# Performance work log

Hardware: AMD Instinct MI355X
Metric: run time of the kernel (lower is better)

## Reference

```python
import jax, jax.numpy as jnp
import numpy as np

N = 50000        # nodes
E = 1_600_000    # edges (avg degree 32)
G = 512          # graphs
F_IN = 9         # node features
H = 64           # hidden dim
ED = 1           # edge feature dim


def _lin(k, fo, fi):
    w = jax.random.normal(k, (fo, fi), jnp.float32) * (1.0 / np.sqrt(fi))
    b = jnp.zeros((fo,), jnp.float32)
    return w, b


def setup_inputs() -> dict:
    key = jax.random.key(0)
    ks = jax.random.split(key, 16)
    x = jax.random.normal(ks[0], (N, F_IN), jnp.float32)
    edge_index = jax.random.randint(ks[1], (2, E), 0, N, dtype=jnp.int64)
    edge_attr = jax.random.normal(ks[2], (E, ED), jnp.float32)
    batch = jnp.sort(jax.random.randint(ks[3], (N,), 0, G, dtype=jnp.int64))
    B_total = jax.random.uniform(ks[4], (G,), jnp.float32) * 100.0
    terminal_mask = jax.random.randint(ks[5], (N,), 0, 2, dtype=jnp.int32)
    c_cost = jax.random.uniform(ks[6], (N,), jnp.float32)
    # conv1: edge lin (ED->F_IN), nn = Linear(F_IN,H), Linear(H,H)
    e1_w, e1_b = _lin(ks[7], F_IN, ED)
    w1a, b1a = _lin(ks[8], H, F_IN)
    w1b, b1b = _lin(ks[9], H, H)
    # conv2: edge lin (ED->H), nn = Linear(H,H), Linear(H,H)
    e2_w, e2_b = _lin(ks[10], H, ED)
    w2a, b2a = _lin(ks[11], H, H)
    w2b, b2b = _lin(ks[12], H, H)
    # readout: Linear(H,H//2), Linear(H//2,1)
    wr1, br1 = _lin(ks[13], H // 2, H)
    wr2, br2 = _lin(ks[14], 1, H // 2)
    return dict(x=x, edge_index=edge_index, edge_attr=edge_attr, batch=batch,
                B_total=B_total, terminal_mask=terminal_mask, c_cost=c_cost,
                e1_w=e1_w, e1_b=e1_b, w1a=w1a, b1a=b1a, w1b=w1b, b1b=b1b,
                e2_w=e2_w, e2_b=e2_b, w2a=w2a, b2a=b2a, w2b=w2b, b2b=b2b,
                wr1=wr1, br1=br1, wr2=wr2, br2=br2)


def _gine(x, src, dst, edge_attr, ew, eb, wa, ba, wb, bb):
    # GINEConv (eps=0): nn(x + sum_j relu(x_j + W_e e_ji))
    e = edge_attr @ ew.T + eb                    # [E, F]
    m = jax.nn.relu(x[src] + e)                  # [E, F] gather + edge fuse
    aggr = jax.ops.segment_sum(m, dst, num_segments=N)  # scatter-add -> [N, F]
    h = x + aggr
    h = jax.nn.relu(h @ wa.T + ba)
    h = jax.nn.relu(h @ wb.T + bb)
    return h


def reference(x, edge_index, edge_attr, batch, B_total, terminal_mask, c_cost,
              e1_w, e1_b, w1a, b1a, w1b, b1b,
              e2_w, e2_b, w2a, b2a, w2b, b2b,
              wr1, br1, wr2, br2):
    src, dst = edge_index[0], edge_index[1]
    h = _gine(x, src, dst, edge_attr, e1_w, e1_b, w1a, b1a, w1b, b1b)
    h = _gine(h, src, dst, edge_attr, e2_w, e2_b, w2a, b2a, w2b, b2b)
    pi_raw = jax.nn.sigmoid((jax.nn.relu(h @ wr1.T + br1) @ wr2.T + br2))[:, 0]
    pi_raw = pi_raw * (1.0 - terminal_mask.astype(jnp.float32))
    node_expenses = pi_raw * c_cost
    total_expenses = jax.ops.segment_sum(node_expenses, batch, num_segments=G)
    ratio = jnp.minimum(B_total[batch] / (total_expenses[batch] + 1e-12), 1.0)
    return pi_raw * ratio
```

## Files before the change

### kernel.cpp

```cpp
#include <hip/hip_runtime.h>
#include <hip/hip_fp16.h>
#include <math.h>

#define N_NODES 50000
#define N_EDGES 1600000
#define N_GRAPHS 512
#define F_IN 9
#define H 64
#define EPB 4096
#define N_SBLK ((N_EDGES + EPB - 1) / EPB)
#define BUCKET_NODES 64
#define N_FBUK ((N_NODES + BUCKET_NODES - 1) / BUCKET_NODES)
#define FCAP 2816

typedef _Float16 f16x8 __attribute__((ext_vector_type(8)));
typedef float f32x4 __attribute__((ext_vector_type(4)));
typedef float f32x2 __attribute__((ext_vector_type(2)));

__device__ __forceinline__ void pack_weights_body(
        const float* __restrict__ w1a, const float* __restrict__ w1b,
        const float* __restrict__ w2a, const float* __restrict__ w2b,
        const float* __restrict__ wr1,
        __half* __restrict__ pk1Ah, __half* __restrict__ pk1Al,
        __half* __restrict__ pk1Bh, __half* __restrict__ pk1Bl,
        __half* __restrict__ pkAh, __half* __restrict__ pkAl,
        __half* __restrict__ pkBh, __half* __restrict__ pkBl,
        __half* __restrict__ pkRh, __half* __restrict__ pkRl) {
    int t = threadIdx.x;
    for (int i = t; i < 2048; i += 512) {
        int j = i & 7, l = (i >> 3) & 63, tt = i >> 9;
        int q = l >> 4, n = l & 15;
        int k = q * 8 + j;
        float v = (k < F_IN) ? w1a[(tt * 16 + n) * F_IN + k] : 0.f;
        __half h = __float2half(v);
        pk1Ah[i] = h; pk1Al[i] = __float2half(v - __half2float(h));
    }
    for (int i = t; i < 4096; i += 512) {
        int j = i & 7, l = (i >> 3) & 63, c = (i >> 9) & 1, tt = i >> 10;
        int q = l >> 4, n = l & 15;
        int src = (tt * 16 + n) * H + c * 32 + q * 8 + j;
        float v1 = w1b[src], wa = w2a[src], wb = w2b[src];
        __half h1 = __float2half(v1), ah = __float2half(wa), bh = __float2half(wb);
        pk1Bh[i] = h1; pk1Bl[i] = __float2half(v1 - __half2float(h1));
        pkAh[i] = ah; pkAl[i] = __float2half(wa - __half2float(ah));
        pkBh[i] = bh; pkBl[i] = __float2half(wb - __half2float(bh));
    }
    for (int i = t; i < 2048; i += 512) {
        int j = i & 7, l = (i >> 3) & 63, c = (i >> 9) & 1, tt = i >> 10;
        int q = l >> 4, n = l & 15;
        float wr = wr1[(tt * 16 + n) * H + c * 32 + q * 8 + j];
        __half rh = __float2half(wr);
        pkRh[i] = rh; pkRl[i] = __float2half(wr - __half2float(rh));
    }
}

__global__ void __launch_bounds__(512)
bucket_scatter(const int* __restrict__ ei,
               const float* __restrict__ ea,
               int* __restrict__ bnext,
               uint2* __restrict__ ebuk,
               const float* __restrict__ w1a,
               const float* __restrict__ w1b,
               const float* __restrict__ w2a,
               const float* __restrict__ w2b,
               const float* __restrict__ wr1,
               __half* pk1Ah, __half* pk1Al,
               __half* pk1Bh, __half* pk1Bl,
               __half* pkAh, __half* pkAl,
               __half* pkBh, __half* pkBl,
               __half* pkRh, __half* pkRl) {
    if (blockIdx.x == 0) {
        pack_weights_body(w1a, w1b, w2a, w2b, wr1, pk1Ah, pk1Al, pk1Bh, pk1Bl,
                          pkAh, pkAl, pkBh, pkBl, pkRh, pkRl);
        return;
    }
    __shared__ int cnt[N_FBUK];
    __shared__ int gbase[N_FBUK];
    for (int i = threadIdx.x; i < N_FBUK; i += 512) cnt[i] = 0;
    __syncthreads();
    int base = (blockIdx.x - 1) * EPB;
    int rk[8];
    unsigned pay[8];
#pragma unroll
    for (int j = 0; j < 8; ++j) {
        int e = base + j * 512 + threadIdx.x;
        rk[j] = -1;
        if (e < N_EDGES) {
            int d = ei[N_EDGES + e];
            int s = ei[e];
            float a = ea[e];
            pay[j] = ((unsigned)s << 16) |
                     (unsigned)__half_as_ushort(__float2half(a));
            int b = d >> 6;
            int r = atomicAdd(&cnt[b], 1);
            rk[j] = (b << 19) | ((d & 63) << 13) | r;
        }
    }
    __syncthreads();
    for (int i = threadIdx.x; i < N_FBUK; i += 512)
        gbase[i] = cnt[i] ? atomicAdd(&bnext[i], cnt[i]) : 0;
    __syncthreads();
#pragma unroll
    for (int j = 0; j < 8; ++j) {
        if (rk[j] < 0) continue;
        int b = rk[j] >> 19, dl = (rk[j] >> 13) & 63, r = rk[j] & 8191;
        int slot = gbase[b] + r;
        if (slot >= FCAP) continue;
        ebuk[(size_t)b * FCAP + slot] = make_uint2(pay[j], (unsigned)dl);
    }
}

#define UNPACK_ATTR(P) __half2float(__ushort_as_half((unsigned short)((P) & 0xffffu)))

__global__ void __launch_bounds__(512)
bucket_fine(const uint2* __restrict__ ebuk,
            const int* __restrict__ bnext,
            unsigned* __restrict__ ep4,
            int* __restrict__ starts, int* __restrict__ deg,
            const float* __restrict__ x,
            const float* __restrict__ e1w,
            const float* __restrict__ e1b,
            float* __restrict__ xs) {
    __shared__ unsigned sorted[FCAP];
    __shared__ int cntN[BUCKET_NODES], offN[BUCKET_NODES], nxtN[BUCKET_NODES];
    int b = blockIdx.x;
    int base = b * FCAP;
    int count = bnext[b];
    if (count > FCAP) count = FCAP;
    int tid = threadIdx.x;
    if (tid < BUCKET_NODES) cntN[tid] = 0;
    __syncthreads();
    uint2 ev[6];
#pragma unroll
    for (int k = 0; k < 6; ++k) {
        int i = tid + k * 512;
        ev[k] = (i < count) ? ebuk[base + i] : make_uint2(0u, 0xFFFFFFFFu);
    }
#pragma unroll
    for (int k = 0; k < 6; ++k)
        if (ev[k].y < (unsigned)BUCKET_NODES) atomicAdd(&cntN[ev[k].y], 1);
    __syncthreads();
    if (tid < 64) {
        int v = cntN[tid];
        int incl = v;
#pragma unroll
        for (int off = 1; off < 64; off <<= 1) {
            int t = __shfl_up(incl, off, 64);
            if (tid >= off) incl += t;
        }
        int excl = incl - v;
        offN[tid] = excl;
        nxtN[tid] = 0;
        int n = (b << 6) + tid;
        if (n < N_NODES) { starts[n] = base + excl; deg[n] = v; }
    }
    __syncthreads();
#pragma unroll
    for (int k = 0; k < 6; ++k) {
        if (ev[k].y < (unsigned)BUCKET_NODES) {
            int r = atomicAdd(&nxtN[ev[k].y], 1);
            sorted[offN[ev[k].y] + r] = ev[k].x;
        }
    }
    __syncthreads();
    for (int i = tid; i < count; i += 512)
        ep4[base + i] = sorted[i];

    int lane = tid & 63, wid = tid >> 6;
    int slot = lane >> 4;
    int f = lane & 15;
    bool act = f < F_IN;
    float wf = act ? e1w[f] : 0.f;
    float bf = act ? e1b[f] : 0.f;
#pragma unroll
    for (int i = 0; i < 8; ++i) {
        int nloc = wid * 8 + i;
        int n = (b << 6) + nloc;
        if (n >= N_NODES) break;
        int off = offN[nloc];
        int dgN = cntN[nloc];
        float acc = 0.f;
        int j = slot;
        for (; j + 12 < dgN; j += 16) {
            unsigned pa = sorted[off + j];
            unsigned pb = sorted[off + j + 4];
            unsigned pc = sorted[off + j + 8];
            unsigned pd = sorted[off + j + 12];
            float xa_ = act ? x[(pa >> 16) * F_IN + f] : 0.f;
            float xb_ = act ? x[(pb >> 16) * F_IN + f] : 0.f;
            float xc_ = act ? x[(pc >> 16) * F_IN + f] : 0.f;
            float xd_ = act ? x[(pd >> 16) * F_IN + f] : 0.f;
            if (act) {
                acc += fmaxf(xa_ + UNPACK_ATTR(pa) * wf + bf, 0.f)
                     + fmaxf(xb_ + UNPACK_ATTR(pb) * wf + bf, 0.f)
                     + fmaxf(xc_ + UNPACK_ATTR(pc) * wf + bf, 0.f)
                     + fmaxf(xd_ + UNPACK_ATTR(pd) * wf + bf, 0.f);
            }
        }
        for (; j < dgN; j += 4) {
            unsigned p = sorted[off + j];
            float xv = act ? x[(p >> 16) * F_IN + f] : 0.f;
            float m = xv + UNPACK_ATTR(p) * wf + bf;
            acc += act ? fmaxf(m, 0.f) : 0.f;
        }
        acc += __shfl_xor(acc, 16, 64);
        acc += __shfl_xor(acc, 32, 64);
        if (lane < 32) {
            float o = (lane < F_IN) ? x[n * F_IN + lane] + acc : 0.f;
            __builtin_nontemporal_store(o, xs + n * 32 + lane);
        }
    }
}

__device__ __forceinline__ void split8(const float* __restrict__ v,
                                       f16x8& hi, f16x8& lo) {
#pragma unroll
    for (int j = 0; j < 8; ++j) {
        _Float16 h = (_Float16)v[j];
        hi[j] = h;
        lo[j] = (_Float16)(v[j] - (float)h);
    }
}

#define TILE3(C, A0H, A0L, A1H, A1L, PH, PL, T) do {                          \
        f16x8 b0h = *(const f16x8*)((PH) + (((T) * 2 + 0) * 64 + lane) * 8);  \
        f16x8 b0l = *(const f16x8*)((PL) + (((T) * 2 + 0) * 64 + lane) * 8);  \
        f16x8 b1h = *(const f16x8*)((PH) + (((T) * 2 + 1) * 64 + lane) * 8);  \
        f16x8 b1l = *(const f16x8*)((PL) + (((T) * 2 + 1) * 64 + lane) * 8);  \
        C = __builtin_amdgcn_mfma_f32_16x16x32_f16(A0H, b0h, C, 0, 0, 0);     \
        C = __builtin_amdgcn_mfma_f32_16x16x32_f16(A0L, b0h, C, 0, 0, 0);     \
        C = __builtin_amdgcn_mfma_f32_16x16x32_f16(A0H, b0l, C, 0, 0, 0);     \
        C = __builtin_amdgcn_mfma_f32_16x16x32_f16(A1H, b1h, C, 0, 0, 0);     \
        C = __builtin_amdgcn_mfma_f32_16x16x32_f16(A1L, b1h, C, 0, 0, 0);     \
        C = __builtin_amdgcn_mfma_f32_16x16x32_f16(A1H, b1l, C, 0, 0, 0);     \
    } while (0)

__global__ void node1_kernel(const float* __restrict__ xs,
                             const __half* __restrict__ pk1Ah, const __half* __restrict__ pk1Al,
                             const float* __restrict__ b1a,
                             const __half* __restrict__ pk1Bh, const __half* __restrict__ pk1Bl,
                             const float* __restrict__ b1b,
                             __half* __restrict__ h1) {
    __shared__ float hbuf[4][16][68];
    int wv = threadIdx.x >> 6;
    int lane = threadIdx.x & 63;
    int gwave = blockIdx.x * 4 + wv;
    bool active = gwave < (N_NODES / 16);
    int base = active ? gwave * 16 : 0;
    int m = lane & 15, q = lane >> 4;
    const _Float16* pAh = (const _Float16*)pk1Ah;
    const _Float16* pAl = (const _Float16*)pk1Al;
    const _Float16* pBh = (const _Float16*)pk1Bh;
    const _Float16* pBl = (const _Float16*)pk1Bl;

    f16x8 ah, al;
    split8(xs + (size_t)(base + m) * 32 + q * 8, ah, al);
#pragma unroll
    for (int t = 0; t < 4; ++t) {
        f32x4 c = {0.f, 0.f, 0.f, 0.f};
        f16x8 bh = *(const f16x8*)(pAh + (t * 64 + lane) * 8);
        f16x8 bl = *(const f16x8*)(pAl + (t * 64 + lane) * 8);
        c = __builtin_amdgcn_mfma_f32_16x16x32_f16(ah, bh, c, 0, 0, 0);
        c = __builtin_amdgcn_mfma_f32_16x16x32_f16(al, bh, c, 0, 0, 0);
        c = __builtin_amdgcn_mfma_f32_16x16x32_f16(ah, bl, c, 0, 0, 0);
        float bias = b1a[t * 16 + m];
#pragma unroll
        for (int r = 0; r < 4; ++r)
            hbuf[wv][q * 4 + r][t * 16 + m] = fmaxf(c[r] + bias, 0.f);
    }
    __syncthreads();
    f16x8 a0h, a0l, a1h, a1l;
    split8(&hbuf[wv][m][q * 8], a0h, a0l);
    split8(&hbuf[wv][m][32 + q * 8], a1h, a1l);
    float tmp[4][4];
#pragma unroll
    for (int t = 0; t < 4; ++t) {
        f32x4 c = {0.f, 0.f, 0.f, 0.f};
        TILE3(c, a0h, a0l, a1h, a1l, pBh, pBl, t);
        float bias = b1b[t * 16 + m];
#pragma unroll
        for (int r = 0; r < 4; ++r)
            tmp[t][r] = fmaxf(c[r] + bias, 0.f);
    }
    __syncthreads();
#pragma unroll
    for (int t = 0; t < 4; ++t)
#pragma unroll
        for (int r = 0; r < 4; ++r)
            hbuf[wv][q * 4 + r][t * 16 + m] = tmp[t][r];
    __syncthreads();
    if (active) {
        int nn = lane >> 2, part = lane & 3;
        f16x8 vlo, vhi;
        const float* rlo = &hbuf[wv][nn][part * 8];
        const float* rhi = &hbuf[wv][nn][32 + part * 8];
#pragma unroll
        for (int j = 0; j < 8; ++j) {
            vlo[j] = (_Float16)rlo[j];
            vhi[j] = (_Float16)rhi[j];
        }
        *(f16x8*)(h1 + (size_t)(base + nn) * 64 + part * 8) = vlo;
        *(f16x8*)(h1 + (size_t)(base + nn) * 64 + 32 + part * 8) = vhi;
    }
}

__global__ void aggphase2_kernel(const __half* __restrict__ h1,
                                 const int* __restrict__ starts,
                                 const int* __restrict__ deg,
                                 const unsigned* __restrict__ ep4,
                                 const float* __restrict__ ew,
                                 const float* __restrict__ eb,
                                 float* __restrict__ htot) {
    int n = blockIdx.x * (blockDim.x >> 6) + (threadIdx.x >> 6);
    int lane = threadIdx.x & 63;
    if (n >= N_NODES) return;
    int q = lane >> 4;
    int l = lane & 15;
    int s0 = starts[n], dg = deg[n];
    const unsigned* ep = ep4 + s0;
    const uint2* h1v = (const uint2*)h1;
    float4 w4 = *(const float4*)(ew + 4 * l);
    float4 b4 = *(const float4*)(eb + 4 * l);
    float a0 = 0.f, a1 = 0.f, a2 = 0.f, a3 = 0.f;
#define EDGE4(P, V) do {                                                   \
        float at = UNPACK_ATTR(P);                                         \
        float2 lo = __half22float2(*(const __half2*)&(V).x);               \
        float2 hi = __half22float2(*(const __half2*)&(V).y);               \
        a0 += fmaxf(lo.x + at * w4.x + b4.x, 0.f);                         \
        a1 += fmaxf(lo.y + at * w4.y + b4.y, 0.f);                         \
        a2 += fmaxf(hi.x + at * w4.z + b4.z, 0.f);                         \
        a3 += fmaxf(hi.y + at * w4.w + b4.w, 0.f);                         \
    } while (0)
    int j = 0;
    for (; j + 16 <= dg; j += 16) {
        unsigned p0 = ep[j + q], p1 = ep[j + 4 + q];
        unsigned p2 = ep[j + 8 + q], p3 = ep[j + 12 + q];
        uint2 v0 = h1v[(size_t)(p0 >> 16) * 16 + l];
        uint2 v1 = h1v[(size_t)(p1 >> 16) * 16 + l];
        uint2 v2 = h1v[(size_t)(p2 >> 16) * 16 + l];
        uint2 v3 = h1v[(size_t)(p3 >> 16) * 16 + l];
        EDGE4(p0, v0); EDGE4(p1, v1); EDGE4(p2, v2); EDGE4(p3, v3);
    }
    for (; j + 4 <= dg; j += 4) {
        unsigned p = ep[j + q];
        uint2 v = h1v[(size_t)(p >> 16) * 16 + l];
        EDGE4(p, v);
    }
    int rem = dg - j;
    if (q < rem) {
        unsigned p = ep[j + q];
        uint2 v = h1v[(size_t)(p >> 16) * 16 + l];
        EDGE4(p, v);
    }
#undef EDGE4
    a0 += __shfl_xor(a0, 16, 64); a0 += __shfl_xor(a0, 32, 64);
    a1 += __shfl_xor(a1, 16, 64); a1 += __shfl_xor(a1, 32, 64);
    a2 += __shfl_xor(a2, 16, 64); a2 += __shfl_xor(a2, 32, 64);
    a3 += __shfl_xor(a3, 16, 64); a3 += __shfl_xor(a3, 32, 64);
    if (q == 0) {
        uint2 sv = h1v[(size_t)n * 16 + l];
        float2 lo = __half22float2(*(const __half2*)&sv.x);
        float2 hi = __half22float2(*(const __half2*)&sv.y);
        f32x4 o;
        o[0] = lo.x + a0; o[1] = lo.y + a1; o[2] = hi.x + a2; o[3] = hi.y + a3;
        __builtin_nontemporal_store(o, (f32x4*)(htot + (size_t)n * 64 + 4 * l));
    }
}

__global__ void node2_kernel(const float* __restrict__ htot,
                             const __half* __restrict__ pkAh, const __half* __restrict__ pkAl,
                             const float* __restrict__ b2a,
                             const __half* __restrict__ pkBh, const __half* __restrict__ pkBl,
                             const float* __restrict__ b2b,
                             const __half* __restrict__ pkRh, const __half* __restrict__ pkRl,
                             const float* __restrict__ br1,
                             const float* __restrict__ wr2,
                             const float* __restrict__ br2,
                             const int* __restrict__ term,
                             const int* __restrict__ batch,
                             const float* __restrict__ ccost,
                             float* __restrict__ pi,
                             float* __restrict__ te) {
    __shared__ float hbuf[4][16][68];
    int wv = threadIdx.x >> 6;
    int lane = threadIdx.x & 63;
    int gwave = blockIdx.x * 4 + wv;
    bool active = gwave < (N_NODES / 16);
    int base = active ? gwave * 16 : 0;
    int m = lane & 15, q = lane >> 4;
    const _Float16* pAh = (const _Float16*)pkAh;
    const _Float16* pAl = (const _Float16*)pkAl;
    const _Float16* pBh = (const _Float16*)pkBh;
    const _Float16* pBl = (const _Float16*)pkBl;
    const _Float16* pRh = (const _Float16*)pkRh;
    const _Float16* pRl = (const _Float16*)pkRl;

    f16x8 a0h, a0l, a1h, a1l;
    {
        const float* hrow = htot + (size_t)(base + m) * 64;
        split8(hrow + q * 8, a0h, a0l);
        split8(hrow + 32 + q * 8, a1h, a1l);
    }
#pragma unroll
    for (int t = 0; t < 4; ++t) {
        f32x4 c = {0.f, 0.f, 0.f, 0.f};
        TILE3(c, a0h, a0l, a1h, a1l, pAh, pAl, t);
        float bias = b2a[t * 16 + m];
#pragma unroll
        for (int r = 0; r < 4; ++r)
            hbuf[wv][q * 4 + r][t * 16 + m] = fmaxf(c[r] + bias, 0.f);
    }
    __syncthreads();
    split8(&hbuf[wv][m][q * 8], a0h, a0l);
    split8(&hbuf[wv][m][32 + q * 8], a1h, a1l);
    float tmp[4][4];
#pragma unroll
    for (int t = 0; t < 4; ++t) {
        f32x4 c = {0.f, 0.f, 0.f, 0.f};
        TILE3(c, a0h, a0l, a1h, a1l, pBh, pBl, t);
        float bias = b2b[t * 16 + m];
#pragma unroll
        for (int r = 0; r < 4; ++r)
            tmp[t][r] = fmaxf(c[r] + bias, 0.f);
    }
    __syncthreads();
#pragma unroll
    for (int t = 0; t < 4; ++t)
#pragma unroll
        for (int r = 0; r < 4; ++r)
            hbuf[wv][q * 4 + r][t * 16 + m] = tmp[t][r];
    __syncthreads();
    split8(&hbuf[wv][m][q * 8], a0h, a0l);
    split8(&hbuf[wv][m][32 + q * 8], a1h, a1l);
    float partial[4] = {0.f, 0.f, 0.f, 0.f};
#pragma unroll
    for (int t = 0; t < 2; ++t) {
        f32x4 c = {0.f, 0.f, 0.f, 0.f};
        TILE3(c, a0h, a0l, a1h, a1l, pRh, pRl, t);
        float bias = br1[t * 16 + m];
        float wv2 = wr2[t * 16 + m];
#pragma unroll
        for (int r = 0; r < 4; ++r)
            partial[r] += fmaxf(c[r] + bias, 0.f) * wv2;
    }
#pragma unroll
    for (int off = 1; off < 16; off <<= 1) {
        partial[0] += __shfl_xor(partial[0], off, 64);
        partial[1] += __shfl_xor(partial[1], off, 64);
        partial[2] += __shfl_xor(partial[2], off, 64);
        partial[3] += __shfl_xor(partial[3], off, 64);
    }
    if (active && m == 0) {
#pragma unroll
        for (int r = 0; r < 4; ++r) {
            int n = base + q * 4 + r;
            float z = partial[r] + br2[0];
            float sig = 1.f / (1.f + expf(-z));
            float pv = sig * (1.f - (float)term[n]);
            pi[n] = pv;
            float contrib = pv * ccost[n];
            if (contrib != 0.f) atomicAdd(&te[batch[n]], contrib);
        }
    }
}

__global__ void final_kernel(const float* __restrict__ pi,
                             const int* __restrict__ batch,
                             const float* __restrict__ Btot,
                             const float* __restrict__ te,
                             float* __restrict__ out) {
    int n = blockIdx.x * blockDim.x + threadIdx.x;
    if (n >= N_NODES) return;
    int b = batch[n];
    float ratio = fminf(Btot[b] / (te[b] + 1e-12f), 1.f);
    out[n] = pi[n] * ratio;
}

extern "C" void kernel_launch(void* const* d_in, const int* in_sizes, int n_in,
                              void* d_out, int out_size, void* d_ws, size_t ws_size,
                              hipStream_t stream) {
    const float* x     = (const float*)d_in[0];
    const int*   ei    = (const int*)d_in[1];
    const float* ea    = (const float*)d_in[2];
    const int*   batch = (const int*)d_in[3];
    const float* Btot  = (const float*)d_in[4];
    const int*   term  = (const int*)d_in[5];
    const float* ccost = (const float*)d_in[6];
    const float* e1w   = (const float*)d_in[7];
    const float* e1b   = (const float*)d_in[8];
    const float* w1a   = (const float*)d_in[9];
    const float* b1a   = (const float*)d_in[10];
    const float* w1b   = (const float*)d_in[11];
    const float* b1b   = (const float*)d_in[12];
    const float* e2w   = (const float*)d_in[13];
    const float* e2b   = (const float*)d_in[14];
    const float* w2a   = (const float*)d_in[15];
    const float* b2a   = (const float*)d_in[16];
    const float* w2b   = (const float*)d_in[17];
    const float* b2b   = (const float*)d_in[18];
    const float* wr1   = (const float*)d_in[19];
    const float* br1   = (const float*)d_in[20];
    const float* wr2   = (const float*)d_in[21];
    const float* br2   = (const float*)d_in[22];

    char* p = (char*)d_ws;
    int*      bnext  = (int*)p;      p += sizeof(int)      * 1024;
    float*    te     = (float*)p;    p += sizeof(float)    * N_GRAPHS;
    int*      starts = (int*)p;      p += sizeof(int)      * N_NODES;
    int*      deg    = (int*)p;      p += sizeof(int)      * N_NODES;
    p = (char*)(((size_t)p + 15) & ~(size_t)15);
    uint2*    ebuk   = (uint2*)p;    p += sizeof(uint2)    * (size_t)N_FBUK * FCAP;
    unsigned* ep4    = (unsigned*)p; p += sizeof(unsigned) * (size_t)N_FBUK * FCAP;
    __half*   h1     = (__half*)p;   p += sizeof(__half)   * (size_t)N_NODES * 64;
    float*    htot   = (float*)p;    p += sizeof(float)    * (size_t)N_NODES * 64;
    float*    xs     = (float*)p;    p += sizeof(float)    * (size_t)N_NODES * 32;
    float*    pi     = (float*)p;    p += sizeof(float)    * N_NODES;
    __half*   pk1Ah  = (__half*)p;   p += sizeof(__half)   * 2048;
    __half*   pk1Al  = (__half*)p;   p += sizeof(__half)   * 2048;
    __half*   pk1Bh  = (__half*)p;   p += sizeof(__half)   * 4096;
    __half*   pk1Bl  = (__half*)p;   p += sizeof(__half)   * 4096;
    __half*   pkAh   = (__half*)p;   p += sizeof(__half)   * 4096;
    __half*   pkAl   = (__half*)p;   p += sizeof(__half)   * 4096;
    __half*   pkBh   = (__half*)p;   p += sizeof(__half)   * 4096;
    __half*   pkBl   = (__half*)p;   p += sizeof(__half)   * 4096;
    __half*   pkRh   = (__half*)p;   p += sizeof(__half)   * 2048;
    __half*   pkRl   = (__half*)p;   p += sizeof(__half)   * 2048;
    float*    out    = (float*)d_out;

    hipMemsetAsync(d_ws, 0, sizeof(int) * 1024 + sizeof(float) * N_GRAPHS, stream);

    bucket_scatter<<<1 + N_SBLK, 512, 0, stream>>>(ei, ea, bnext, ebuk,
                                                   w1a, w1b, w2a, w2b, wr1,
                                                   pk1Ah, pk1Al, pk1Bh, pk1Bl,
                                                   pkAh, pkAl, pkBh, pkBl, pkRh, pkRl);
    bucket_fine<<<N_FBUK, 512, 0, stream>>>(ebuk, bnext, ep4, starts, deg,
                                            x, e1w, e1b, xs);
    node1_kernel<<<(N_NODES / 16 + 3) / 4, 256, 0, stream>>>(xs, pk1Ah, pk1Al, b1a,
                                                             pk1Bh, pk1Bl, b1b, h1);
    aggphase2_kernel<<<(N_NODES + 3) / 4, 256, 0, stream>>>(h1, starts, deg, ep4,
                                                            e2w, e2b, htot);
    node2_kernel<<<(N_NODES / 16 + 3) / 4, 256, 0, stream>>>(htot,
                                                             pkAh, pkAl, b2a,
                                                             pkBh, pkBl, b2b,
                                                             pkRh, pkRl, br1,
                                                             wr2, br2, term,
                                                             batch, ccost, pi, te);
    final_kernel<<<(N_NODES + 255) / 256, 256, 0, stream>>>(pi, batch, Btot, te, out);
}
```

Measured before the change: 218.9 us.

## Fuse layer-1 node MLP into bucket_fine kernel via LDS staging

```diff
diff --git a/kernel.cpp b/kernel.cpp
--- a/kernel.cpp
+++ b/kernel.cpp
@@ -112,6 +112,29 @@
 
 #define UNPACK_ATTR(P) __half2float(__ushort_as_half((unsigned short)((P) & 0xffffu)))
 
+__device__ __forceinline__ void split8(const float* __restrict__ v,
+                                       f16x8& hi, f16x8& lo) {
+#pragma unroll
+    for (int j = 0; j < 8; ++j) {
+        _Float16 h = (_Float16)v[j];
+        hi[j] = h;
+        lo[j] = (_Float16)(v[j] - (float)h);
+    }
+}
+
+#define TILE3(C, A0H, A0L, A1H, A1L, PH, PL, T) do {                          \
+        f16x8 b0h = *(const f16x8*)((PH) + (((T) * 2 + 0) * 64 + lane) * 8);  \
+        f16x8 b0l = *(const f16x8*)((PL) + (((T) * 2 + 0) * 64 + lane) * 8);  \
+        f16x8 b1h = *(const f16x8*)((PH) + (((T) * 2 + 1) * 64 + lane) * 8);  \
+        f16x8 b1l = *(const f16x8*)((PL) + (((T) * 2 + 1) * 64 + lane) * 8);  \
+        C = __builtin_amdgcn_mfma_f32_16x16x32_f16(A0H, b0h, C, 0, 0, 0);     \
+        C = __builtin_amdgcn_mfma_f32_16x16x32_f16(A0L, b0h, C, 0, 0, 0);     \
+        C = __builtin_amdgcn_mfma_f32_16x16x32_f16(A0H, b0l, C, 0, 0, 0);     \
+        C = __builtin_amdgcn_mfma_f32_16x16x32_f16(A1H, b1h, C, 0, 0, 0);     \
+        C = __builtin_amdgcn_mfma_f32_16x16x32_f16(A1L, b1h, C, 0, 0, 0);     \
+        C = __builtin_amdgcn_mfma_f32_16x16x32_f16(A1H, b1l, C, 0, 0, 0);     \
+    } while (0)
+
 __global__ void __launch_bounds__(512)
 bucket_fine(const uint2* __restrict__ ebuk,
             const int* __restrict__ bnext,
@@ -120,9 +143,15 @@
             const float* __restrict__ x,
             const float* __restrict__ e1w,
             const float* __restrict__ e1b,
-            float* __restrict__ xs) {
+            const __half* __restrict__ pk1Ah, const __half* __restrict__ pk1Al,
+            const float* __restrict__ b1a,
+            const __half* __restrict__ pk1Bh, const __half* __restrict__ pk1Bl,
+            const float* __restrict__ b1b,
+            __half* __restrict__ h1) {
     __shared__ unsigned sorted[FCAP];
     __shared__ int cntN[BUCKET_NODES], offN[BUCKET_NODES], nxtN[BUCKET_NODES];
+    __shared__ float xs_lds[BUCKET_NODES][32];
+    __shared__ float hbuf[4][16][68];
     int b = blockIdx.x;
     int base = b * FCAP;
     int count = bnext[b];
@@ -176,9 +205,9 @@
     for (int i = 0; i < 8; ++i) {
         int nloc = wid * 8 + i;
         int n = (b << 6) + nloc;
-        if (n >= N_NODES) break;
+        bool valid = (n < N_NODES);
         int off = offN[nloc];
-        int dgN = cntN[nloc];
+        int dgN = valid ? cntN[nloc] : 0;
         float acc = 0.f;
         int j = slot;
         for (; j + 12 < dgN; j += 16) {
@@ -206,101 +235,71 @@
         acc += __shfl_xor(acc, 16, 64);
         acc += __shfl_xor(acc, 32, 64);
         if (lane < 32) {
-            float o = (lane < F_IN) ? x[n * F_IN + lane] + acc : 0.f;
-            __builtin_nontemporal_store(o, xs + n * 32 + lane);
-        }
-    }
-}
-
-__device__ __forceinline__ void split8(const float* __restrict__ v,
-                                       f16x8& hi, f16x8& lo) {
-#pragma unroll
-    for (int j = 0; j < 8; ++j) {
-        _Float16 h = (_Float16)v[j];
-        hi[j] = h;
-        lo[j] = (_Float16)(v[j] - (float)h);
-    }
-}
-
-#define TILE3(C, A0H, A0L, A1H, A1L, PH, PL, T) do {                          \
-        f16x8 b0h = *(const f16x8*)((PH) + (((T) * 2 + 0) * 64 + lane) * 8);  \
-        f16x8 b0l = *(const f16x8*)((PL) + (((T) * 2 + 0) * 64 + lane) * 8);  \
-        f16x8 b1h = *(const f16x8*)((PH) + (((T) * 2 + 1) * 64 + lane) * 8);  \
-        f16x8 b1l = *(const f16x8*)((PL) + (((T) * 2 + 1) * 64 + lane) * 8);  \
-        C = __builtin_amdgcn_mfma_f32_16x16x32_f16(A0H, b0h, C, 0, 0, 0);     \
-        C = __builtin_amdgcn_mfma_f32_16x16x32_f16(A0L, b0h, C, 0, 0, 0);     \
-        C = __builtin_amdgcn_mfma_f32_16x16x32_f16(A0H, b0l, C, 0, 0, 0);     \
-        C = __builtin_amdgcn_mfma_f32_16x16x32_f16(A1H, b1h, C, 0, 0, 0);     \
-        C = __builtin_amdgcn_mfma_f32_16x16x32_f16(A1L, b1h, C, 0, 0, 0);     \
-        C = __builtin_amdgcn_mfma_f32_16x16x32_f16(A1H, b1l, C, 0, 0, 0);     \
-    } while (0)
-
-__global__ void node1_kernel(const float* __restrict__ xs,
-                             const __half* __restrict__ pk1Ah, const __half* __restrict__ pk1Al,
-                             const float* __restrict__ b1a,
-                             const __half* __restrict__ pk1Bh, const __half* __restrict__ pk1Bl,
-                             const float* __restrict__ b1b,
-                             __half* __restrict__ h1) {
-    __shared__ float hbuf[4][16][68];
-    int wv = threadIdx.x >> 6;
-    int lane = threadIdx.x & 63;
-    int gwave = blockIdx.x * 4 + wv;
-    bool active = gwave < (N_NODES / 16);
-    int base = active ? gwave * 16 : 0;
+            float o = 0.f;
+            if (valid && lane < F_IN) o = x[n * F_IN + lane] + acc;
+            xs_lds[nloc][lane] = o;
+        }
+    }
+    __syncthreads();
+
+    bool mlpw = (wid < 4);
     int m = lane & 15, q = lane >> 4;
     const _Float16* pAh = (const _Float16*)pk1Ah;
     const _Float16* pAl = (const _Float16*)pk1Al;
     const _Float16* pBh = (const _Float16*)pk1Bh;
     const _Float16* pBl = (const _Float16*)pk1Bl;
-
-    f16x8 ah, al;
-    split8(xs + (size_t)(base + m) * 32 + q * 8, ah, al);
-#pragma unroll
-    for (int t = 0; t < 4; ++t) {
-        f32x4 c = {0.f, 0.f, 0.f, 0.f};
-        f16x8 bh = *(const f16x8*)(pAh + (t * 64 + lane) * 8);
-        f16x8 bl = *(const f16x8*)(pAl + (t * 64 + lane) * 8);
-        c = __builtin_amdgcn_mfma_f32_16x16x32_f16(ah, bh, c, 0, 0, 0);
-        c = __builtin_amdgcn_mfma_f32_16x16x32_f16(al, bh, c, 0, 0, 0);
-        c = __builtin_amdgcn_mfma_f32_16x16x32_f16(ah, bl, c, 0, 0, 0);
-        float bias = b1a[t * 16 + m];
-#pragma unroll
-        for (int r = 0; r < 4; ++r)
-            hbuf[wv][q * 4 + r][t * 16 + m] = fmaxf(c[r] + bias, 0.f);
-    }
-    __syncthreads();
-    f16x8 a0h, a0l, a1h, a1l;
-    split8(&hbuf[wv][m][q * 8], a0h, a0l);
-    split8(&hbuf[wv][m][32 + q * 8], a1h, a1l);
-    float tmp[4][4];
-#pragma unroll
-    for (int t = 0; t < 4; ++t) {
-        f32x4 c = {0.f, 0.f, 0.f, 0.f};
-        TILE3(c, a0h, a0l, a1h, a1l, pBh, pBl, t);
-        float bias = b1b[t * 16 + m];
-#pragma unroll
-        for (int r = 0; r < 4; ++r)
-            tmp[t][r] = fmaxf(c[r] + bias, 0.f);
-    }
-    __syncthreads();
-#pragma unroll
-    for (int t = 0; t < 4; ++t)
-#pragma unroll
-        for (int r = 0; r < 4; ++r)
-            hbuf[wv][q * 4 + r][t * 16 + m] = tmp[t][r];
-    __syncthreads();
-    if (active) {
+    if (mlpw) {
+        f16x8 ah, al;
+        split8(&xs_lds[wid * 16 + m][q * 8], ah, al);
+#pragma unroll
+        for (int t = 0; t < 4; ++t) {
+            f32x4 c = {0.f, 0.f, 0.f, 0.f};
+            f16x8 bh = *(const f16x8*)(pAh + (t * 64 + lane) * 8);
+            f16x8 bl = *(const f16x8*)(pAl + (t * 64 + lane) * 8);
+            c = __builtin_amdgcn_mfma_f32_16x16x32_f16(ah, bh, c, 0, 0, 0);
+            c = __builtin_amdgcn_mfma_f32_16x16x32_f16(al, bh, c, 0, 0, 0);
+            c = __builtin_amdgcn_mfma_f32_16x16x32_f16(ah, bl, c, 0, 0, 0);
+            float bias = b1a[t * 16 + m];
+#pragma unroll
+            for (int r = 0; r < 4; ++r)
+                hbuf[wid][q * 4 + r][t * 16 + m] = fmaxf(c[r] + bias, 0.f);
+        }
+    }
+    __syncthreads();
+    if (mlpw) {
+        f16x8 a0h, a0l, a1h, a1l;
+        split8(&hbuf[wid][m][q * 8], a0h, a0l);
+        split8(&hbuf[wid][m][32 + q * 8], a1h, a1l);
+        float tmp[4][4];
+#pragma unroll
+        for (int t = 0; t < 4; ++t) {
+            f32x4 c = {0.f, 0.f, 0.f, 0.f};
+            TILE3(c, a0h, a0l, a1h, a1l, pBh, pBl, t);
+            float bias = b1b[t * 16 + m];
+#pragma unroll
+            for (int r = 0; r < 4; ++r)
+                tmp[t][r] = fmaxf(c[r] + bias, 0.f);
+        }
+        __builtin_amdgcn_s_barrier();
+#pragma unroll
+        for (int t = 0; t < 4; ++t)
+#pragma unroll
+            for (int r = 0; r < 4; ++r)
+                hbuf[wid][q * 4 + r][t * 16 + m] = tmp[t][r];
         int nn = lane >> 2, part = lane & 3;
-        f16x8 vlo, vhi;
-        const float* rlo = &hbuf[wv][nn][part * 8];
-        const float* rhi = &hbuf[wv][nn][32 + part * 8];
-#pragma unroll
-        for (int j = 0; j < 8; ++j) {
-            vlo[j] = (_Float16)rlo[j];
-            vhi[j] = (_Float16)rhi[j];
-        }
-        *(f16x8*)(h1 + (size_t)(base + nn) * 64 + part * 8) = vlo;
-        *(f16x8*)(h1 + (size_t)(base + nn) * 64 + 32 + part * 8) = vhi;
+        int n = (b << 6) + wid * 16 + nn;
+        if (n < N_NODES) {
+            f16x8 vlo, vhi;
+            const float* rlo = &hbuf[wid][nn][part * 8];
+            const float* rhi = &hbuf[wid][nn][32 + part * 8];
+#pragma unroll
+            for (int j = 0; j < 8; ++j) {
+                vlo[j] = (_Float16)rlo[j];
+                vhi[j] = (_Float16)rhi[j];
+            }
+            *(f16x8*)(h1 + (size_t)n * 64 + part * 8) = vlo;
+            *(f16x8*)(h1 + (size_t)n * 64 + 32 + part * 8) = vhi;
+        }
     }
 }
 
@@ -513,7 +512,6 @@
     unsigned* ep4    = (unsigned*)p; p += sizeof(unsigned) * (size_t)N_FBUK * FCAP;
     __half*   h1     = (__half*)p;   p += sizeof(__half)   * (size_t)N_NODES * 64;
     float*    htot   = (float*)p;    p += sizeof(float)    * (size_t)N_NODES * 64;
-    float*    xs     = (float*)p;    p += sizeof(float)    * (size_t)N_NODES * 32;
     float*    pi     = (float*)p;    p += sizeof(float)    * N_NODES;
     __half*   pk1Ah  = (__half*)p;   p += sizeof(__half)   * 2048;
     __half*   pk1Al  = (__half*)p;   p += sizeof(__half)   * 2048;
@@ -534,9 +532,8 @@
                                                    pk1Ah, pk1Al, pk1Bh, pk1Bl,
                                                    pkAh, pkAl, pkBh, pkBl, pkRh, pkRl);
     bucket_fine<<<N_FBUK, 512, 0, stream>>>(ebuk, bnext, ep4, starts, deg,
-                                            x, e1w, e1b, xs);
-    node1_kernel<<<(N_NODES / 16 + 3) / 4, 256, 0, stream>>>(xs, pk1Ah, pk1Al, b1a,
-                                                             pk1Bh, pk1Bl, b1b, h1);
+                                            x, e1w, e1b,
+                                            pk1Ah, pk1Al, b1a, pk1Bh, pk1Bl, b1b, h1);
     aggphase2_kernel<<<(N_NODES + 3) / 4, 256, 0, stream>>>(h1, starts, deg, ep4,
                                                             e2w, e2b, htot);
     node2_kernel<<<(N_NODES / 16 + 3) / 4, 256, 0, stream>>>(htot,
```

Measured after the change: 217.3 us. No clear change (-0.7%).
